# Kernel optimization log

Measured on AMD Instinct MI355X. Metric: run time of the kernel, lower is better.

The kernel has to match this reference:

```python
import jax, jax.numpy as jnp
import numpy as np

N_NODES = 100000
N_EDGES = 1600000
IN_FEATS = 128
HID = 32
N_REL = 5
N_BASES = 2
N_PAIRS = 4096


def setup_inputs() -> dict:
    key = jax.random.key(0)
    ks = jax.random.split(key, 24)
    d = {}
    d['x'] = jax.random.normal(ks[0], (N_NODES, IN_FEATS), dtype=jnp.float32)
    d['edge_mask'] = jnp.ones((N_EDGES,), dtype=jnp.float32)
    d['etype'] = jax.random.randint(ks[1], (N_EDGES,), 0, N_REL, dtype=jnp.int32)
    d['src'] = jax.random.randint(ks[2], (N_EDGES,), 0, N_NODES, dtype=jnp.int32)
    d['dst'] = jax.random.randint(ks[3], (N_EDGES,), 0, N_NODES, dtype=jnp.int32)
    d['users_idx'] = jax.random.randint(ks[4], (N_PAIRS,), 0, N_NODES, dtype=jnp.int32)
    d['items_idx'] = jax.random.randint(ks[5], (N_PAIRS,), 0, N_NODES, dtype=jnp.int32)
    # RelGraphConv params (basis decomposition): layer1 in->32, layers 2,3 32->32
    def s(k, din):
        return 1.0 / np.sqrt(din)
    d['V1'] = jax.random.normal(ks[6], (N_BASES, IN_FEATS, HID), dtype=jnp.float32) * s(0, IN_FEATS)
    d['comp1'] = jax.random.normal(ks[7], (N_REL, N_BASES), dtype=jnp.float32)
    d['loop1'] = jax.random.normal(ks[8], (IN_FEATS, HID), dtype=jnp.float32) * s(0, IN_FEATS)
    d['b1'] = jnp.zeros((HID,), dtype=jnp.float32)
    d['V2'] = jax.random.normal(ks[9], (N_BASES, HID, HID), dtype=jnp.float32) * s(0, HID)
    d['comp2'] = jax.random.normal(ks[10], (N_REL, N_BASES), dtype=jnp.float32)
    d['loop2'] = jax.random.normal(ks[11], (HID, HID), dtype=jnp.float32) * s(0, HID)
    d['b2'] = jnp.zeros((HID,), dtype=jnp.float32)
    d['V3'] = jax.random.normal(ks[12], (N_BASES, HID, HID), dtype=jnp.float32) * s(0, HID)
    d['comp3'] = jax.random.normal(ks[13], (N_REL, N_BASES), dtype=jnp.float32)
    d['loop3'] = jax.random.normal(ks[14], (HID, HID), dtype=jnp.float32) * s(0, HID)
    d['b3'] = jnp.zeros((HID,), dtype=jnp.float32)
    # MLP head: lin1 (2*sum(latent_dim[1:]) = 192 -> 128), lin2 (128 -> 1)
    d['w1'] = jax.random.normal(ks[15], (2 * 3 * HID, 128), dtype=jnp.float32) * (1.0 / np.sqrt(2 * 3 * HID))
    d['bw1'] = jnp.zeros((128,), dtype=jnp.float32)
    d['w2'] = jax.random.normal(ks[16], (128, 1), dtype=jnp.float32) * (1.0 / np.sqrt(128))
    d['bw2'] = jnp.zeros((1,), dtype=jnp.float32)
    return d


def _rgcn_layer(x, V, comp, loopw, bias, etype, src, dst, norm):
    # basis-decomposed relational conv: W_r = sum_b comp[r,b] * V[b]
    xb = jnp.einsum('nd,bdo->nbo', x, V)                       # [N,B,O]
    msg = jnp.einsum('eb,ebo->eo', comp[etype], xb[src])       # [E,O]
    msg = msg * norm[:, None]                                  # edge_mask norm
    agg = jax.ops.segment_sum(msg, dst, num_segments=x.shape[0])
    return jnp.tanh(agg + x @ loopw + bias)


def reference(x, edge_mask, etype, src, dst, users_idx, items_idx,
              V1, comp1, loop1, b1, V2, comp2, loop2, b2, V3, comp3, loop3, b3,
              w1, bw1, w2, bw2):
    h1 = _rgcn_layer(x, V1, comp1, loop1, b1, etype, src, dst, edge_mask)
    h2 = _rgcn_layer(h1, V2, comp2, loop2, b2, etype, src, dst, edge_mask)
    h3 = _rgcn_layer(h2, V3, comp3, loop3, b3, etype, src, dst, edge_mask)
    concat_states = jnp.concatenate([h1, h2, h3], axis=1)      # [N, 96]
    feats = jnp.concatenate([concat_states[users_idx], concat_states[items_idx]], axis=1)  # [P,192]
    hidden = jax.nn.relu(feats @ w1 + bw1)
    out = hidden @ w2 + bw2
    return out[:, 0]  # multiply_by = 1
```

## Files before the change

### kernel.cpp

```cpp
#include <hip/hip_runtime.h>
#include <stdint.h>

#define N_NODES  100000
#define N_EDGES  1600000
#define IN_FEATS 128
#define HID      32
#define N_REL    5
#define N_BASES  2
#define N_PAIRS  4096

#define NB        196
#define BCAP      16384
#define EPB       2048
#define SC_BLOCKS 782
#define NGROUPS   6250

typedef __attribute__((ext_vector_type(8))) short short8;
typedef __attribute__((ext_vector_type(4))) float f32x4;

__device__ inline unsigned int pack_bf16(float a, float b) {
    unsigned int ua = __float_as_uint(a), ub = __float_as_uint(b);
    ua = (ua + 0x7fffu + ((ua >> 16) & 1u)) >> 16;
    ub = (ub + 0x7fffu + ((ub >> 16) & 1u)) >> 16;
    return ua | (ub << 16);
}

__device__ inline unsigned short bf16_1(float a) {
    unsigned int u = __float_as_uint(a);
    u = (u + 0x7fffu + ((u >> 16) & 1u)) >> 16;
    return (unsigned short)u;
}


__global__ __launch_bounds__(256) void k_pre(
    const float* __restrict__ V1, const float* __restrict__ comp1, const float* __restrict__ loop1,
    const float* __restrict__ V2, const float* __restrict__ comp2, const float* __restrict__ loop2,
    const float* __restrict__ V3, const float* __restrict__ comp3, const float* __restrict__ loop3,
    unsigned short* __restrict__ Wbf1, unsigned short* __restrict__ Wbf2,
    unsigned short* __restrict__ Wbf3,
    const int* __restrict__ src, const int* __restrict__ dst,
    const int* __restrict__ etype, const float* __restrict__ mask,
    int* __restrict__ gcur, int2* __restrict__ ebuf) {
    int b = blockIdx.x;
    int t = threadIdx.x;
    if (b < 144) {
        const float *V, *comp, *loopw;
        unsigned short* Wbf;
        int D, idx;
        if (b < 96)      { V = V1; comp = comp1; loopw = loop1; Wbf = Wbf1; D = IN_FEATS; idx = b * 256 + t; }
        else if (b < 120){ V = V2; comp = comp2; loopw = loop2; Wbf = Wbf2; D = HID;      idx = (b - 96) * 256 + t; }
        else             { V = V3; comp = comp3; loopw = loop3; Wbf = Wbf3; D = HID;      idx = (b - 120) * 256 + t; }
        if (idx >= 192 * D) return;
        int j = idx / D, k = idx % D;
        float v;
        if (j < 160) {
            int r = j >> 5, o = j & 31;
            v = comp[r * 2 + 0] * V[(size_t)(0 * D + k) * 32 + o]
              + comp[r * 2 + 1] * V[(size_t)(1 * D + k) * 32 + o];
        } else {
            v = loopw[k * 32 + (j - 160)];
        }
        Wbf[idx] = bf16_1(v);
        return;
    }
    __shared__ int lh[NB];
    __shared__ int lex[NB];
    __shared__ int gbase[NB];
    __shared__ int scanbuf[256];
    __shared__ int2  srec[EPB];
    __shared__ short sb[EPB];
    int blk = b - 144;
    int e0 = blk * EPB;
    if (t < NB) lh[t] = 0;
    __syncthreads();
    int2 rec[8];
    int  bk[8];
#pragma unroll
    for (int i = 0; i < 8; i++) {
        int e = e0 + t + i * 256;
        if (e < N_EDGES) {
            int d = dst[e];
            bk[i] = d >> 9;
            rec[i].x = ((d & 511) << 23) | (src[e] * 80 + etype[e] * 16);
            rec[i].y = __float_as_int(mask[e]);
            atomicAdd(&lh[bk[i]], 1);
        } else bk[i] = -1;
    }
    __syncthreads();
    int cnt = (t < NB) ? lh[t] : 0;
    scanbuf[t] = cnt;
    __syncthreads();
    for (int off = 1; off < 256; off <<= 1) {
        int v = (t >= off) ? scanbuf[t - off] : 0;
        __syncthreads();
        scanbuf[t] += v;
        __syncthreads();
    }
    if (t < NB) {
        lex[t] = scanbuf[t] - cnt;
        gbase[t] = t * BCAP + (cnt ? atomicAdd(&gcur[t], cnt) : 0);
        lh[t] = 0;
    }
    __syncthreads();
#pragma unroll
    for (int i = 0; i < 8; i++) {
        if (bk[i] >= 0) {
            int p = lex[bk[i]] + atomicAdd(&lh[bk[i]], 1);
            srec[p] = rec[i];
            sb[p] = (short)bk[i];
        }
    }
    __syncthreads();
    int total = scanbuf[NB - 1];
    for (int idx = t; idx < total; idx += 256) {
        int bb = sb[idx];
        ebuf[gbase[bb] + (idx - lex[bb])] = srec[idx];
    }
}


__global__ __launch_bounds__(512) void k_bsort2(
    const int* __restrict__ gcur, const int2* __restrict__ ebuf,
    int2* __restrict__ esort, int* __restrict__ offsets) {
    __shared__ int hist[512];
    __shared__ int incl[512];
    __shared__ int cur[512];
    __shared__ int bs[256];
    __shared__ int sBase, sCnt;
    int blk = blockIdx.x, b = blk >> 1, h = blk & 1, t = threadIdx.x;
    if (t < 256) bs[t] = (t < NB) ? gcur[t] : 0;
    __syncthreads();
    for (int off = 1; off < 256; off <<= 1) {
        int v = 0;
        if (t < 256 && t >= off) v = bs[t - off];
        __syncthreads();
        if (t < 256) bs[t] += v;
        __syncthreads();
    }
    if (t == 0) { sCnt = gcur[b]; sBase = bs[b] - gcur[b]; }
    hist[t] = 0;
    __syncthreads();
    int cnt = sCnt, gbase = sBase;
    const int2* slab = ebuf + (size_t)b * BCAP;
    for (int e = t; e < cnt; e += 512) {
        int dl = ((unsigned)slab[e].x) >> 23;
        atomicAdd(&hist[dl], 1);
    }
    __syncthreads();
    incl[t] = hist[t];
    __syncthreads();
    for (int off = 1; off < 512; off <<= 1) {
        int v = 0;
        if (t >= off) v = incl[t - off];
        __syncthreads();
        incl[t] += v;
        __syncthreads();
    }
    int ex = incl[t] - hist[t];
    cur[t] = ex;
    if ((t >> 8) == h) {
        int n = (b << 9) + t;
        if (n <= N_NODES) offsets[n] = gbase + ex;
    }
    if (b == NB - 1 && h == 1 && t == 0) offsets[N_NODES] = N_EDGES;
    __syncthreads();
    for (int e = t; e < cnt; e += 512) {
        int2 pk = slab[e];
        int dl = ((unsigned)pk.x) >> 23;
        if ((dl >> 8) == h) {
            int pos = gbase + atomicAdd(&cur[dl], 1);
            int2 rec;
            rec.x = pk.x & 0x7fffff;
            rec.y = pk.y;
            esort[pos] = rec;
        }
    }
}


__global__ __launch_bounds__(256) void k_transform_l1(
    const float* __restrict__ xin,
    const unsigned short* __restrict__ Wbf, const float* __restrict__ bias,
    unsigned short* __restrict__ xs16, float* __restrict__ aggout) {
    __shared__ unsigned short As[16 * 136];
    int t = threadIdx.x;
    int wv = t >> 6, lane = t & 63;
    int q = lane >> 4, n16 = lane & 15;
    short8 bfr[3][4];
#pragma unroll
    for (int i = 0; i < 3; i++) {
        int tt = wv * 3 + i;
#pragma unroll
        for (int ks = 0; ks < 4; ks++)
            bfr[i][ks] = *(const short8*)(Wbf + (tt * 16 + n16) * 128 + ks * 32 + q * 8);
    }
    float bv0 = bias[n16], bv1 = bias[16 + n16];
    int node_l = t >> 4;
    int seg    = t & 15;
    int g0 = blockIdx.x * 5;
    float4 p0, p1;
    {
        const float* xr = xin + ((size_t)(g0 * 16 + node_l)) * 128 + seg * 8;
        p0 = *(const float4*)xr;
        p1 = *(const float4*)(xr + 4);
    }
    for (int gi = 0; gi < 5; gi++) {
        int g = g0 + gi;
        int n0 = g * 16;
        __syncthreads();
        {
            unsigned int u0 = pack_bf16(p0.x, p0.y);
            unsigned int u1 = pack_bf16(p0.z, p0.w);
            unsigned int u2 = pack_bf16(p1.x, p1.y);
            unsigned int u3 = pack_bf16(p1.z, p1.w);
            uint4 v; v.x = u0; v.y = u1; v.z = u2; v.w = u3;
            *(uint4*)(As + node_l * 136 + seg * 8) = v;
        }
        __syncthreads();
        if (gi + 1 < 5) {
            const float* xr = xin + ((size_t)((g + 1) * 16 + node_l)) * 128 + seg * 8;
            p0 = *(const float4*)xr;
            p1 = *(const float4*)(xr + 4);
        }
        short8 afr[4];
#pragma unroll
        for (int ks = 0; ks < 4; ks++)
            afr[ks] = *(const short8*)(As + n16 * 136 + ks * 32 + q * 8);
        f32x4 d[3];
        f32x4 z = {0.f, 0.f, 0.f, 0.f};
#pragma unroll
        for (int i = 0; i < 3; i++) d[i] = z;
#pragma unroll
        for (int i = 0; i < 3; i++)
#pragma unroll
            for (int ks = 0; ks < 4; ks++)
                d[i] = __builtin_amdgcn_mfma_f32_16x16x32_bf16(afr[ks], bfr[i][ks], d[i], 0, 0, 0);
#pragma unroll
        for (int i = 0; i < 3; i++) {
            int tt = wv * 3 + i;
            if (tt < 10) {
#pragma unroll
                for (int r = 0; r < 4; r++) {
                    int node = n0 + q * 4 + r;
                    xs16[(size_t)node * 160 + tt * 16 + n16] = bf16_1(d[i][r]);
                }
            } else {
                float bv = (tt == 10) ? bv0 : bv1;
                int o = (tt - 10) * 16 + n16;
#pragma unroll
                for (int r = 0; r < 4; r++) {
                    int node = n0 + q * 4 + r;
                    aggout[(size_t)node * 32 + o] = d[i][r] + bv;
                }
            }
        }
    }
}


__global__ __launch_bounds__(256) void k_transform_reg32(
    const float* __restrict__ xin, int xstride,
    const unsigned short* __restrict__ Wbf, const float* __restrict__ bias,
    unsigned short* __restrict__ xs16, float* __restrict__ aggout) {
    int t = threadIdx.x;
    int wv = t >> 6, lane = t & 63;
    int q = lane >> 4, n16 = lane & 15;
    short8 bfr[12];
#pragma unroll
    for (int t12 = 0; t12 < 12; t12++)
        bfr[t12] = *(const short8*)(Wbf + (t12 * 16 + n16) * 32 + q * 8);
    float bv0 = bias[n16], bv1 = bias[16 + n16];
    int gstep = gridDim.x * 4;
    int g = blockIdx.x * 4 + wv;
    float4 x0, x1;
    if (g < NGROUPS) {
        const float* xr = xin + (size_t)(g * 16 + n16) * xstride + q * 8;
        x0 = *(const float4*)(xr);
        x1 = *(const float4*)(xr + 4);
    }
    while (g < NGROUPS) {
        int gn = g + gstep;
        union { unsigned int u[4]; short8 s; } cv;
        cv.u[0] = pack_bf16(x0.x, x0.y);
        cv.u[1] = pack_bf16(x0.z, x0.w);
        cv.u[2] = pack_bf16(x1.x, x1.y);
        cv.u[3] = pack_bf16(x1.z, x1.w);
        short8 afr = cv.s;
        float4 nx0, nx1;
        if (gn < NGROUPS) {
            const float* xr = xin + (size_t)(gn * 16 + n16) * xstride + q * 8;
            nx0 = *(const float4*)(xr);
            nx1 = *(const float4*)(xr + 4);
        }
        f32x4 d[12];
        f32x4 z = {0.f, 0.f, 0.f, 0.f};
#pragma unroll
        for (int i = 0; i < 12; i++) d[i] = z;
#pragma unroll
        for (int t12 = 0; t12 < 12; t12++)
            d[t12] = __builtin_amdgcn_mfma_f32_16x16x32_bf16(afr, bfr[t12], d[t12], 0, 0, 0);
        int n0 = g * 16;
#pragma unroll
        for (int t12 = 0; t12 < 10; t12++) {
#pragma unroll
            for (int r = 0; r < 4; r++) {
                int node = n0 + q * 4 + r;
                xs16[(size_t)node * 160 + t12 * 16 + n16] = bf16_1(d[t12][r]);
            }
        }
#pragma unroll
        for (int r = 0; r < 4; r++) {
            int node = n0 + q * 4 + r;
            aggout[(size_t)node * 32 + n16]      = d[10][r] + bv0;
            aggout[(size_t)node * 32 + 16 + n16] = d[11][r] + bv1;
        }
        x0 = nx0; x1 = nx1; g = gn;
    }
}


__global__ __launch_bounds__(256) void k_agg(
    const int* __restrict__ offsets, const int2* __restrict__ esort,
    const unsigned int* __restrict__ xrel16, const float* __restrict__ agg,
    float* __restrict__ hout, int hoff) {
    int v = blockIdx.x * 32 + (threadIdx.x >> 3);
    int o = threadIdx.x & 7;
    if (v >= N_NODES) return;
    int s0 = offsets[v], s1 = offsets[v + 1];
    float4 a0 = *(const float4*)(agg + (size_t)v * 32 + o * 4);
    float acc0 = a0.x, acc1 = a0.y, acc2 = a0.z, acc3 = a0.w;
    int last = s1 - 1;
    for (int e = s0; e < s1; e += 16) {
        int addr[16];
        float m[16];
#pragma unroll
        for (int i = 0; i < 16; i++) {
            int ei = e + i;
            int ec = (ei <= last) ? ei : last;
            int2 pk = esort[ec];
            addr[i] = pk.x;
            m[i] = (ei <= last) ? __int_as_float(pk.y) : 0.f;
        }
        uint2 xw[16];
#pragma unroll
        for (int i = 0; i < 16; i++)
            xw[i] = *(const uint2*)(xrel16 + (unsigned)addr[i] + o * 2);
#pragma unroll
        for (int i = 0; i < 16; i++) {
            float f0 = __uint_as_float(xw[i].x << 16);
            float f1 = __uint_as_float(xw[i].x & 0xffff0000u);
            float f2 = __uint_as_float(xw[i].y << 16);
            float f3 = __uint_as_float(xw[i].y & 0xffff0000u);
            acc0 = fmaf(m[i], f0, acc0);
            acc1 = fmaf(m[i], f1, acc1);
            acc2 = fmaf(m[i], f2, acc2);
            acc3 = fmaf(m[i], f3, acc3);
        }
    }
    float4 r;
    r.x = tanhf(acc0); r.y = tanhf(acc1); r.z = tanhf(acc2); r.w = tanhf(acc3);
    *(float4*)(hout + (size_t)v * 96 + hoff + o * 4) = r;
}


__global__ void k_mlp(const float* __restrict__ concat, const int* __restrict__ uidx,
                      const int* __restrict__ iidx,
                      const float* __restrict__ w1, const float* __restrict__ bw1,
                      const float* __restrict__ w2, const float* __restrict__ bw2,
                      float* __restrict__ out) {
    __shared__ float feats[192];
    __shared__ float red[2];
    int p = blockIdx.x;
    int t = threadIdx.x;
    int u = uidx[p], it = iidx[p];
    for (int k = t; k < 192; k += 128)
        feats[k] = (k < 96) ? concat[(size_t)u * 96 + k] : concat[(size_t)it * 96 + (k - 96)];
    __syncthreads();
    float acc = bw1[t];
    for (int k = 0; k < 192; k++) acc += feats[k] * w1[k * 128 + t];
    float h = fmaxf(acc, 0.f);
    float part = h * w2[t];
    for (int off = 32; off > 0; off >>= 1) part += __shfl_down(part, off, 64);
    if ((t & 63) == 0) red[t >> 6] = part;
    __syncthreads();
    if (t == 0) out[p] = red[0] + red[1] + bw2[0];
}


extern "C" void kernel_launch(void* const* d_in, const int* in_sizes, int n_in,
                              void* d_out, int out_size, void* d_ws, size_t ws_size,
                              hipStream_t stream) {
    const float* x         = (const float*)d_in[0];
    const float* edge_mask = (const float*)d_in[1];
    const int*   etype     = (const int*)d_in[2];
    const int*   src       = (const int*)d_in[3];
    const int*   dst       = (const int*)d_in[4];
    const int*   users_idx = (const int*)d_in[5];
    const int*   items_idx = (const int*)d_in[6];
    const float* V1        = (const float*)d_in[7];
    const float* comp1     = (const float*)d_in[8];
    const float* loop1     = (const float*)d_in[9];
    const float* b1        = (const float*)d_in[10];
    const float* V2        = (const float*)d_in[11];
    const float* comp2     = (const float*)d_in[12];
    const float* loop2     = (const float*)d_in[13];
    const float* b2        = (const float*)d_in[14];
    const float* V3        = (const float*)d_in[15];
    const float* comp3     = (const float*)d_in[16];
    const float* loop3     = (const float*)d_in[17];
    const float* b3        = (const float*)d_in[18];
    const float* w1        = (const float*)d_in[19];
    const float* bw1       = (const float*)d_in[20];
    const float* w2        = (const float*)d_in[21];
    const float* bw2       = (const float*)d_in[22];
    float* out = (float*)d_out;

    uintptr_t w = (uintptr_t)d_ws;
    auto al = [&](size_t bytes) { uintptr_t p = (w + 255) & ~(uintptr_t)255; w = p + bytes; return p; };
    int*   gcur    = (int*)al(sizeof(int) * NB);
    int*   offsets = (int*)al(sizeof(int) * (N_NODES + 1));
    int2*  ebuf    = (int2*)al(sizeof(int2) * (size_t)NB * BCAP);
    unsigned int* xrel16 = (unsigned int*)al(sizeof(unsigned int) * (size_t)N_NODES * 80);
    int2*  esort   = (int2*)al(sizeof(int2) * N_EDGES);
    unsigned short* Wbf1 = (unsigned short*)al(sizeof(unsigned short) * 192 * IN_FEATS);
    unsigned short* Wbf2 = (unsigned short*)al(sizeof(unsigned short) * 192 * HID);
    unsigned short* Wbf3 = (unsigned short*)al(sizeof(unsigned short) * 192 * HID);
    float* agg     = (float*)al(sizeof(float) * (size_t)N_NODES * 32);
    float* concat  = (float*)al(sizeof(float) * (size_t)N_NODES * 96);

    hipMemsetAsync(gcur, 0, sizeof(int) * NB, stream);

    k_pre<<<144 + SC_BLOCKS, 256, 0, stream>>>(V1, comp1, loop1, V2, comp2, loop2,
                                               V3, comp3, loop3, Wbf1, Wbf2, Wbf3,
                                               src, dst, etype, edge_mask, gcur, ebuf);
    k_bsort2<<<2 * NB, 512, 0, stream>>>(gcur, ebuf, esort, offsets);

    const int agrid = (N_NODES + 31) / 32;

    k_transform_l1<<<1250, 256, 0, stream>>>(x, Wbf1, b1, (unsigned short*)xrel16, agg);
    k_agg<<<agrid, 256, 0, stream>>>(offsets, esort, xrel16, agg, concat, 0);

    k_transform_reg32<<<784, 256, 0, stream>>>(concat + 0, 96, Wbf2, b2, (unsigned short*)xrel16, agg);
    k_agg<<<agrid, 256, 0, stream>>>(offsets, esort, xrel16, agg, concat, 32);

    k_transform_reg32<<<784, 256, 0, stream>>>(concat + 32, 96, Wbf3, b3, (unsigned short*)xrel16, agg);
    k_agg<<<agrid, 256, 0, stream>>>(offsets, esort, xrel16, agg, concat, 64);

    k_mlp<<<N_PAIRS, 128, 0, stream>>>(concat, users_idx, items_idx, w1, bw1, w2, bw2, out);
}
```

Measured before the change: 356.8 us.

## Fuse next-layer transform into aggregation and merge L1 transform with edge bucketing

Result: faster. 345.6 us (-3.1%).

```diff
diff --git a/kernel.cpp b/kernel.cpp
--- a/kernel.cpp
+++ b/kernel.cpp
@@ -13,6 +13,7 @@
 #define BCAP      16384
 #define EPB       2048
 #define SC_BLOCKS 782
+#define TL1_BLOCKS 1250
 #define NGROUPS   6250
 
 typedef __attribute__((ext_vector_type(8))) short short8;
@@ -32,89 +33,171 @@
 }
 
 
-__global__ __launch_bounds__(256) void k_pre(
+__global__ __launch_bounds__(256) void k_wprep(
     const float* __restrict__ V1, const float* __restrict__ comp1, const float* __restrict__ loop1,
     const float* __restrict__ V2, const float* __restrict__ comp2, const float* __restrict__ loop2,
     const float* __restrict__ V3, const float* __restrict__ comp3, const float* __restrict__ loop3,
     unsigned short* __restrict__ Wbf1, unsigned short* __restrict__ Wbf2,
-    unsigned short* __restrict__ Wbf3,
+    unsigned short* __restrict__ Wbf3, int* __restrict__ gcur) {
+    int b = blockIdx.x;
+    int t = threadIdx.x;
+    if (b == 0 && t < NB) gcur[t] = 0;
+    const float *V, *comp, *loopw;
+    unsigned short* Wbf;
+    int D, idx;
+    if (b < 96)      { V = V1; comp = comp1; loopw = loop1; Wbf = Wbf1; D = IN_FEATS; idx = b * 256 + t; }
+    else if (b < 120){ V = V2; comp = comp2; loopw = loop2; Wbf = Wbf2; D = HID;      idx = (b - 96) * 256 + t; }
+    else             { V = V3; comp = comp3; loopw = loop3; Wbf = Wbf3; D = HID;      idx = (b - 120) * 256 + t; }
+    if (idx >= 192 * D) return;
+    int j = idx / D, k = idx % D;
+    float v;
+    if (j < 160) {
+        int r = j >> 5, o = j & 31;
+        v = comp[r * 2 + 0] * V[(size_t)(0 * D + k) * 32 + o]
+          + comp[r * 2 + 1] * V[(size_t)(1 * D + k) * 32 + o];
+    } else {
+        v = loopw[k * 32 + (j - 160)];
+    }
+    Wbf[idx] = bf16_1(v);
+}
+
+
+__global__ __launch_bounds__(256) void k_fused1(
     const int* __restrict__ src, const int* __restrict__ dst,
     const int* __restrict__ etype, const float* __restrict__ mask,
-    int* __restrict__ gcur, int2* __restrict__ ebuf) {
+    int* __restrict__ gcur, int2* __restrict__ ebuf,
+    const float* __restrict__ xin,
+    const unsigned short* __restrict__ Wbf, const float* __restrict__ bias,
+    unsigned short* __restrict__ xs16, float* __restrict__ aggout) {
     int b = blockIdx.x;
     int t = threadIdx.x;
-    if (b < 144) {
-        const float *V, *comp, *loopw;
-        unsigned short* Wbf;
-        int D, idx;
-        if (b < 96)      { V = V1; comp = comp1; loopw = loop1; Wbf = Wbf1; D = IN_FEATS; idx = b * 256 + t; }
-        else if (b < 120){ V = V2; comp = comp2; loopw = loop2; Wbf = Wbf2; D = HID;      idx = (b - 96) * 256 + t; }
-        else             { V = V3; comp = comp3; loopw = loop3; Wbf = Wbf3; D = HID;      idx = (b - 120) * 256 + t; }
-        if (idx >= 192 * D) return;
-        int j = idx / D, k = idx % D;
-        float v;
-        if (j < 160) {
-            int r = j >> 5, o = j & 31;
-            v = comp[r * 2 + 0] * V[(size_t)(0 * D + k) * 32 + o]
-              + comp[r * 2 + 1] * V[(size_t)(1 * D + k) * 32 + o];
-        } else {
-            v = loopw[k * 32 + (j - 160)];
-        }
-        Wbf[idx] = bf16_1(v);
+    if (b < SC_BLOCKS) {
+        __shared__ int lh[NB];
+        __shared__ int lex[NB];
+        __shared__ int gbase[NB];
+        __shared__ int scanbuf[256];
+        __shared__ int2  srec[EPB];
+        __shared__ short sb[EPB];
+        int e0 = b * EPB;
+        if (t < NB) lh[t] = 0;
+        __syncthreads();
+        int2 rec[8];
+        int  bk[8];
+#pragma unroll
+        for (int i = 0; i < 8; i++) {
+            int e = e0 + t + i * 256;
+            if (e < N_EDGES) {
+                int d = dst[e];
+                bk[i] = d >> 9;
+                rec[i].x = ((d & 511) << 23) | (src[e] * 80 + etype[e] * 16);
+                rec[i].y = __float_as_int(mask[e]);
+                atomicAdd(&lh[bk[i]], 1);
+            } else bk[i] = -1;
+        }
+        __syncthreads();
+        int cnt = (t < NB) ? lh[t] : 0;
+        scanbuf[t] = cnt;
+        __syncthreads();
+        for (int off = 1; off < 256; off <<= 1) {
+            int v = (t >= off) ? scanbuf[t - off] : 0;
+            __syncthreads();
+            scanbuf[t] += v;
+            __syncthreads();
+        }
+        if (t < NB) {
+            lex[t] = scanbuf[t] - cnt;
+            gbase[t] = t * BCAP + (cnt ? atomicAdd(&gcur[t], cnt) : 0);
+            lh[t] = 0;
+        }
+        __syncthreads();
+#pragma unroll
+        for (int i = 0; i < 8; i++) {
+            if (bk[i] >= 0) {
+                int p = lex[bk[i]] + atomicAdd(&lh[bk[i]], 1);
+                srec[p] = rec[i];
+                sb[p] = (short)bk[i];
+            }
+        }
+        __syncthreads();
+        int total = scanbuf[NB - 1];
+        for (int idx = t; idx < total; idx += 256) {
+            int bb = sb[idx];
+            ebuf[gbase[bb] + (idx - lex[bb])] = srec[idx];
+        }
         return;
     }
-    __shared__ int lh[NB];
-    __shared__ int lex[NB];
-    __shared__ int gbase[NB];
-    __shared__ int scanbuf[256];
-    __shared__ int2  srec[EPB];
-    __shared__ short sb[EPB];
-    int blk = b - 144;
-    int e0 = blk * EPB;
-    if (t < NB) lh[t] = 0;
-    __syncthreads();
-    int2 rec[8];
-    int  bk[8];
-#pragma unroll
-    for (int i = 0; i < 8; i++) {
-        int e = e0 + t + i * 256;
-        if (e < N_EDGES) {
-            int d = dst[e];
-            bk[i] = d >> 9;
-            rec[i].x = ((d & 511) << 23) | (src[e] * 80 + etype[e] * 16);
-            rec[i].y = __float_as_int(mask[e]);
-            atomicAdd(&lh[bk[i]], 1);
-        } else bk[i] = -1;
-    }
-    __syncthreads();
-    int cnt = (t < NB) ? lh[t] : 0;
-    scanbuf[t] = cnt;
-    __syncthreads();
-    for (int off = 1; off < 256; off <<= 1) {
-        int v = (t >= off) ? scanbuf[t - off] : 0;
-        __syncthreads();
-        scanbuf[t] += v;
-        __syncthreads();
-    }
-    if (t < NB) {
-        lex[t] = scanbuf[t] - cnt;
-        gbase[t] = t * BCAP + (cnt ? atomicAdd(&gcur[t], cnt) : 0);
-        lh[t] = 0;
-    }
-    __syncthreads();
-#pragma unroll
-    for (int i = 0; i < 8; i++) {
-        if (bk[i] >= 0) {
-            int p = lex[bk[i]] + atomicAdd(&lh[bk[i]], 1);
-            srec[p] = rec[i];
-            sb[p] = (short)bk[i];
-        }
-    }
-    __syncthreads();
-    int total = scanbuf[NB - 1];
-    for (int idx = t; idx < total; idx += 256) {
-        int bb = sb[idx];
-        ebuf[gbase[bb] + (idx - lex[bb])] = srec[idx];
+    __shared__ unsigned short As[16 * 136];
+    int bb = b - SC_BLOCKS;
+    int wv = t >> 6, lane = t & 63;
+    int q = lane >> 4, n16 = lane & 15;
+    short8 bfr[3][4];
+#pragma unroll
+    for (int i = 0; i < 3; i++) {
+        int tt = wv * 3 + i;
+#pragma unroll
+        for (int ks = 0; ks < 4; ks++)
+            bfr[i][ks] = *(const short8*)(Wbf + (tt * 16 + n16) * 128 + ks * 32 + q * 8);
+    }
+    float bv0 = bias[n16], bv1 = bias[16 + n16];
+    int node_l = t >> 4;
+    int seg    = t & 15;
+    int g0 = bb * 5;
+    float4 p0, p1;
+    {
+        const float* xr = xin + ((size_t)(g0 * 16 + node_l)) * 128 + seg * 8;
+        p0 = *(const float4*)xr;
+        p1 = *(const float4*)(xr + 4);
+    }
+    for (int gi = 0; gi < 5; gi++) {
+        int g = g0 + gi;
+        int n0 = g * 16;
+        __syncthreads();
+        {
+            unsigned int u0 = pack_bf16(p0.x, p0.y);
+            unsigned int u1 = pack_bf16(p0.z, p0.w);
+            unsigned int u2 = pack_bf16(p1.x, p1.y);
+            unsigned int u3 = pack_bf16(p1.z, p1.w);
+            uint4 v; v.x = u0; v.y = u1; v.z = u2; v.w = u3;
+            *(uint4*)(As + node_l * 136 + seg * 8) = v;
+        }
+        __syncthreads();
+        if (gi + 1 < 5) {
+            const float* xr = xin + ((size_t)((g + 1) * 16 + node_l)) * 128 + seg * 8;
+            p0 = *(const float4*)xr;
+            p1 = *(const float4*)(xr + 4);
+        }
+        short8 afr[4];
+#pragma unroll
+        for (int ks = 0; ks < 4; ks++)
+            afr[ks] = *(const short8*)(As + n16 * 136 + ks * 32 + q * 8);
+        f32x4 d[3];
+        f32x4 z = {0.f, 0.f, 0.f, 0.f};
+#pragma unroll
+        for (int i = 0; i < 3; i++) d[i] = z;
+#pragma unroll
+        for (int i = 0; i < 3; i++)
+#pragma unroll
+            for (int ks = 0; ks < 4; ks++)
+                d[i] = __builtin_amdgcn_mfma_f32_16x16x32_bf16(afr[ks], bfr[i][ks], d[i], 0, 0, 0);
+#pragma unroll
+        for (int i = 0; i < 3; i++) {
+            int tt = wv * 3 + i;
+            if (tt < 10) {
+#pragma unroll
+                for (int r = 0; r < 4; r++) {
+                    int node = n0 + q * 4 + r;
+                    xs16[(size_t)node * 160 + tt * 16 + n16] = bf16_1(d[i][r]);
+                }
+            } else {
+                float bv = (tt == 10) ? bv0 : bv1;
+                int o = (tt - 10) * 16 + n16;
+#pragma unroll
+                for (int r = 0; r < 4; r++) {
+                    int node = n0 + q * 4 + r;
+                    aggout[(size_t)node * 32 + o] = d[i][r] + bv;
+                }
+            }
+        }
     }
 }
 
@@ -178,143 +261,90 @@
 }
 
 
-__global__ __launch_bounds__(256) void k_transform_l1(
-    const float* __restrict__ xin,
+__global__ __launch_bounds__(256) void k_agg_t(
+    const int* __restrict__ offsets, const int2* __restrict__ esort,
+    const unsigned int* __restrict__ xrel16, const float* __restrict__ agg,
+    float* __restrict__ hout, int hoff,
     const unsigned short* __restrict__ Wbf, const float* __restrict__ bias,
-    unsigned short* __restrict__ xs16, float* __restrict__ aggout) {
-    __shared__ unsigned short As[16 * 136];
+    unsigned short* __restrict__ xs16_out, float* __restrict__ agg_out) {
+    __shared__ unsigned int hbf[32][20];
     int t = threadIdx.x;
+    int nl = t >> 3;
+    int v = blockIdx.x * 32 + nl;
+    int o = t & 7;
+    int s0 = offsets[v], s1 = offsets[v + 1];
+    float4 a0 = *(const float4*)(agg + (size_t)v * 32 + o * 4);
+    float acc0 = a0.x, acc1 = a0.y, acc2 = a0.z, acc3 = a0.w;
+    int last = s1 - 1;
+    for (int e = s0; e < s1; e += 16) {
+        int addr[16];
+        float m[16];
+#pragma unroll
+        for (int i = 0; i < 16; i++) {
+            int ei = e + i;
+            int ec = (ei <= last) ? ei : last;
+            int2 pk = esort[ec];
+            addr[i] = pk.x;
+            m[i] = (ei <= last) ? __int_as_float(pk.y) : 0.f;
+        }
+        uint2 xw[16];
+#pragma unroll
+        for (int i = 0; i < 16; i++)
+            xw[i] = *(const uint2*)(xrel16 + (unsigned)addr[i] + o * 2);
+#pragma unroll
+        for (int i = 0; i < 16; i++) {
+            float f0 = __uint_as_float(xw[i].x << 16);
+            float f1 = __uint_as_float(xw[i].x & 0xffff0000u);
+            float f2 = __uint_as_float(xw[i].y << 16);
+            float f3 = __uint_as_float(xw[i].y & 0xffff0000u);
+            acc0 = fmaf(m[i], f0, acc0);
+            acc1 = fmaf(m[i], f1, acc1);
+            acc2 = fmaf(m[i], f2, acc2);
+            acc3 = fmaf(m[i], f3, acc3);
+        }
+    }
+    float4 r;
+    r.x = tanhf(acc0); r.y = tanhf(acc1); r.z = tanhf(acc2); r.w = tanhf(acc3);
+    *(float4*)(hout + (size_t)v * 96 + hoff + o * 4) = r;
+    hbf[nl][o * 2]     = pack_bf16(r.x, r.y);
+    hbf[nl][o * 2 + 1] = pack_bf16(r.z, r.w);
+    __syncthreads();
     int wv = t >> 6, lane = t & 63;
     int q = lane >> 4, n16 = lane & 15;
-    short8 bfr[3][4];
-#pragma unroll
-    for (int i = 0; i < 3; i++) {
-        int tt = wv * 3 + i;
-#pragma unroll
-        for (int ks = 0; ks < 4; ks++)
-            bfr[i][ks] = *(const short8*)(Wbf + (tt * 16 + n16) * 128 + ks * 32 + q * 8);
-    }
+    int gg = wv & 1;
+    int tbase = (wv >> 1) * 6;
+    short8 afr = *(const short8*)&hbf[gg * 16 + n16][q * 4];
+    short8 bfr[6];
+#pragma unroll
+    for (int j = 0; j < 6; j++)
+        bfr[j] = *(const short8*)(Wbf + ((tbase + j) * 16 + n16) * 32 + q * 8);
+    f32x4 d[6];
+    f32x4 z = {0.f, 0.f, 0.f, 0.f};
+#pragma unroll
+    for (int j = 0; j < 6; j++) d[j] = z;
+#pragma unroll
+    for (int j = 0; j < 6; j++)
+        d[j] = __builtin_amdgcn_mfma_f32_16x16x32_bf16(afr, bfr[j], d[j], 0, 0, 0);
     float bv0 = bias[n16], bv1 = bias[16 + n16];
-    int node_l = t >> 4;
-    int seg    = t & 15;
-    int g0 = blockIdx.x * 5;
-    float4 p0, p1;
-    {
-        const float* xr = xin + ((size_t)(g0 * 16 + node_l)) * 128 + seg * 8;
-        p0 = *(const float4*)xr;
-        p1 = *(const float4*)(xr + 4);
-    }
-    for (int gi = 0; gi < 5; gi++) {
-        int g = g0 + gi;
-        int n0 = g * 16;
-        __syncthreads();
-        {
-            unsigned int u0 = pack_bf16(p0.x, p0.y);
-            unsigned int u1 = pack_bf16(p0.z, p0.w);
-            unsigned int u2 = pack_bf16(p1.x, p1.y);
-            unsigned int u3 = pack_bf16(p1.z, p1.w);
-            uint4 v; v.x = u0; v.y = u1; v.z = u2; v.w = u3;
-            *(uint4*)(As + node_l * 136 + seg * 8) = v;
-        }
-        __syncthreads();
-        if (gi + 1 < 5) {
-            const float* xr = xin + ((size_t)((g + 1) * 16 + node_l)) * 128 + seg * 8;
-            p0 = *(const float4*)xr;
-            p1 = *(const float4*)(xr + 4);
-        }
-        short8 afr[4];
-#pragma unroll
-        for (int ks = 0; ks < 4; ks++)
-            afr[ks] = *(const short8*)(As + n16 * 136 + ks * 32 + q * 8);
-        f32x4 d[3];
-        f32x4 z = {0.f, 0.f, 0.f, 0.f};
-#pragma unroll
-        for (int i = 0; i < 3; i++) d[i] = z;
-#pragma unroll
-        for (int i = 0; i < 3; i++)
-#pragma unroll
-            for (int ks = 0; ks < 4; ks++)
-                d[i] = __builtin_amdgcn_mfma_f32_16x16x32_bf16(afr[ks], bfr[i][ks], d[i], 0, 0, 0);
-#pragma unroll
-        for (int i = 0; i < 3; i++) {
-            int tt = wv * 3 + i;
-            if (tt < 10) {
-#pragma unroll
-                for (int r = 0; r < 4; r++) {
-                    int node = n0 + q * 4 + r;
-                    xs16[(size_t)node * 160 + tt * 16 + n16] = bf16_1(d[i][r]);
-                }
-            } else {
-                float bv = (tt == 10) ? bv0 : bv1;
-                int o = (tt - 10) * 16 + n16;
-#pragma unroll
-                for (int r = 0; r < 4; r++) {
-                    int node = n0 + q * 4 + r;
-                    aggout[(size_t)node * 32 + o] = d[i][r] + bv;
-                }
+    int n0 = blockIdx.x * 32 + gg * 16;
+#pragma unroll
+    for (int j = 0; j < 6; j++) {
+        int tt = tbase + j;
+        if (tt < 10) {
+#pragma unroll
+            for (int rr = 0; rr < 4; rr++) {
+                int node = n0 + q * 4 + rr;
+                xs16_out[(size_t)node * 160 + tt * 16 + n16] = bf16_1(d[j][rr]);
             }
-        }
-    }
-}
-
-
-__global__ __launch_bounds__(256) void k_transform_reg32(
-    const float* __restrict__ xin, int xstride,
-    const unsigned short* __restrict__ Wbf, const float* __restrict__ bias,
-    unsigned short* __restrict__ xs16, float* __restrict__ aggout) {
-    int t = threadIdx.x;
-    int wv = t >> 6, lane = t & 63;
-    int q = lane >> 4, n16 = lane & 15;
-    short8 bfr[12];
-#pragma unroll
-    for (int t12 = 0; t12 < 12; t12++)
-        bfr[t12] = *(const short8*)(Wbf + (t12 * 16 + n16) * 32 + q * 8);
-    float bv0 = bias[n16], bv1 = bias[16 + n16];
-    int gstep = gridDim.x * 4;
-    int g = blockIdx.x * 4 + wv;
-    float4 x0, x1;
-    if (g < NGROUPS) {
-        const float* xr = xin + (size_t)(g * 16 + n16) * xstride + q * 8;
-        x0 = *(const float4*)(xr);
-        x1 = *(const float4*)(xr + 4);
-    }
-    while (g < NGROUPS) {
-        int gn = g + gstep;
-        union { unsigned int u[4]; short8 s; } cv;
-        cv.u[0] = pack_bf16(x0.x, x0.y);
-        cv.u[1] = pack_bf16(x0.z, x0.w);
-        cv.u[2] = pack_bf16(x1.x, x1.y);
-        cv.u[3] = pack_bf16(x1.z, x1.w);
-        short8 afr = cv.s;
-        float4 nx0, nx1;
-        if (gn < NGROUPS) {
-            const float* xr = xin + (size_t)(gn * 16 + n16) * xstride + q * 8;
-            nx0 = *(const float4*)(xr);
-            nx1 = *(const float4*)(xr + 4);
-        }
-        f32x4 d[12];
-        f32x4 z = {0.f, 0.f, 0.f, 0.f};
-#pragma unroll
-        for (int i = 0; i < 12; i++) d[i] = z;
-#pragma unroll
-        for (int t12 = 0; t12 < 12; t12++)
-            d[t12] = __builtin_amdgcn_mfma_f32_16x16x32_bf16(afr, bfr[t12], d[t12], 0, 0, 0);
-        int n0 = g * 16;
-#pragma unroll
-        for (int t12 = 0; t12 < 10; t12++) {
-#pragma unroll
-            for (int r = 0; r < 4; r++) {
-                int node = n0 + q * 4 + r;
-                xs16[(size_t)node * 160 + t12 * 16 + n16] = bf16_1(d[t12][r]);
+        } else {
+            float bv = (tt == 10) ? bv0 : bv1;
+            int oo = (tt - 10) * 16 + n16;
+#pragma unroll
+            for (int rr = 0; rr < 4; rr++) {
+                int node = n0 + q * 4 + rr;
+                agg_out[(size_t)node * 32 + oo] = d[j][rr] + bv;
             }
         }
-#pragma unroll
-        for (int r = 0; r < 4; r++) {
-            int node = n0 + q * 4 + r;
-            aggout[(size_t)node * 32 + n16]      = d[10][r] + bv0;
-            aggout[(size_t)node * 32 + 16 + n16] = d[11][r] + bv1;
-        }
-        x0 = nx0; x1 = nx1; g = gn;
     }
 }
 
@@ -420,31 +450,30 @@
     int*   gcur    = (int*)al(sizeof(int) * NB);
     int*   offsets = (int*)al(sizeof(int) * (N_NODES + 1));
     int2*  ebuf    = (int2*)al(sizeof(int2) * (size_t)NB * BCAP);
-    unsigned int* xrel16 = (unsigned int*)al(sizeof(unsigned int) * (size_t)N_NODES * 80);
+    unsigned int* xrelA = (unsigned int*)al(sizeof(unsigned int) * (size_t)N_NODES * 80);
+    unsigned int* xrelB = (unsigned int*)al(sizeof(unsigned int) * (size_t)N_NODES * 80);
     int2*  esort   = (int2*)al(sizeof(int2) * N_EDGES);
     unsigned short* Wbf1 = (unsigned short*)al(sizeof(unsigned short) * 192 * IN_FEATS);
     unsigned short* Wbf2 = (unsigned short*)al(sizeof(unsigned short) * 192 * HID);
     unsigned short* Wbf3 = (unsigned short*)al(sizeof(unsigned short) * 192 * HID);
-    float* agg     = (float*)al(sizeof(float) * (size_t)N_NODES * 32);
+    float* aggA    = (float*)al(sizeof(float) * (size_t)N_NODES * 32);
+    float* aggB    = (float*)al(sizeof(float) * (size_t)N_NODES * 32);
     float* concat  = (float*)al(sizeof(float) * (size_t)N_NODES * 96);
 
-    hipMemsetAsync(gcur, 0, sizeof(int) * NB, stream);
-
-    k_pre<<<144 + SC_BLOCKS, 256, 0, stream>>>(V1, comp1, loop1, V2, comp2, loop2,
-                                               V3, comp3, loop3, Wbf1, Wbf2, Wbf3,
-                                               src, dst, etype, edge_mask, gcur, ebuf);
+    k_wprep<<<144, 256, 0, stream>>>(V1, comp1, loop1, V2, comp2, loop2,
+                                     V3, comp3, loop3, Wbf1, Wbf2, Wbf3, gcur);
+    k_fused1<<<SC_BLOCKS + TL1_BLOCKS, 256, 0, stream>>>(
+        src, dst, etype, edge_mask, gcur, ebuf,
+        x, Wbf1, b1, (unsigned short*)xrelA, aggA);
     k_bsort2<<<2 * NB, 512, 0, stream>>>(gcur, ebuf, esort, offsets);
 
-    const int agrid = (N_NODES + 31) / 32;
-
-    k_transform_l1<<<1250, 256, 0, stream>>>(x, Wbf1, b1, (unsigned short*)xrel16, agg);
-    k_agg<<<agrid, 256, 0, stream>>>(offsets, esort, xrel16, agg, concat, 0);
-
-    k_transform_reg32<<<784, 256, 0, stream>>>(concat + 0, 96, Wbf2, b2, (unsigned short*)xrel16, agg);
-    k_agg<<<agrid, 256, 0, stream>>>(offsets, esort, xrel16, agg, concat, 32);
-
-    k_transform_reg32<<<784, 256, 0, stream>>>(concat + 32, 96, Wbf3, b3, (unsigned short*)xrel16, agg);
-    k_agg<<<agrid, 256, 0, stream>>>(offsets, esort, xrel16, agg, concat, 64);
+    const int agrid = N_NODES / 32;
+
+    k_agg_t<<<agrid, 256, 0, stream>>>(offsets, esort, xrelA, aggA, concat, 0,
+                                       Wbf2, b2, (unsigned short*)xrelB, aggB);
+    k_agg_t<<<agrid, 256, 0, stream>>>(offsets, esort, xrelB, aggB, concat, 32,
+                                       Wbf3, b3, (unsigned short*)xrelA, aggA);
+    k_agg<<<agrid, 256, 0, stream>>>(offsets, esort, xrelA, aggA, concat, 64);
 
     k_mlp<<<N_PAIRS, 128, 0, stream>>>(concat, users_idx, items_idx, w1, bw1, w2, bw2, out);
 }
```
